# Kernel tuning notes

Hardware: AMD Instinct MI355X
Metric: run time of the kernel (lower is better)

Reference implementation:

```python
import jax, jax.numpy as jnp
import numpy as np
import math

IN_DIM = 3
WIDTH = 256
DEPTH = 6
OUT_DIM = 1
W0_FIRST = 30.0
W0_HIDDEN = 1.0
N_POINTS = 1048576


def _uniform(key, shape, bound):
    return jax.random.uniform(key, shape, dtype=jnp.float32, minval=-bound, maxval=bound)


def setup_inputs() -> dict:
    key = jax.random.key(0)
    ks = jax.random.split(key, 8)
    xyt = jax.random.uniform(ks[0], (N_POINTS, IN_DIM), dtype=jnp.float32, minval=-1.0, maxval=1.0)
    # first layer: bound = 1/in_features
    W0 = _uniform(ks[1], (WIDTH, IN_DIM), 1.0 / IN_DIM)
    b0 = jnp.zeros((WIDTH,), jnp.float32)
    # hidden layers: bound = sqrt(6/width)/w0_hidden
    hb = math.sqrt(6.0 / WIDTH) / W0_HIDDEN
    W1 = _uniform(ks[2], (WIDTH, WIDTH), hb)
    b1 = jnp.zeros((WIDTH,), jnp.float32)
    W2 = _uniform(ks[3], (WIDTH, WIDTH), hb)
    b2 = jnp.zeros((WIDTH,), jnp.float32)
    W3 = _uniform(ks[4], (WIDTH, WIDTH), hb)
    b3 = jnp.zeros((WIDTH,), jnp.float32)
    W4 = _uniform(ks[5], (WIDTH, WIDTH), hb)
    b4 = jnp.zeros((WIDTH,), jnp.float32)
    Wf = _uniform(ks[6], (OUT_DIM, WIDTH), hb)
    bf = jnp.zeros((OUT_DIM,), jnp.float32)
    return {"xyt": xyt, "W0": W0, "b0": b0, "W1": W1, "b1": b1,
            "W2": W2, "b2": b2, "W3": W3, "b3": b3, "W4": W4, "b4": b4,
            "Wf": Wf, "bf": bf}


def reference(xyt, W0, b0, W1, b1, W2, b2, W3, b3, W4, b4, Wf, bf):
    # SineLayer: sin(w0 * (x @ W^T + b)); torch Linear weight is [out, in]
    h = jnp.sin(W0_FIRST * (xyt @ W0.T + b0))          # [N, 256]
    for W, b in ((W1, b1), (W2, b2), (W3, b3), (W4, b4)):
        h = jnp.sin(W0_HIDDEN * (h @ W.T + b))          # [N, 256]
    out = h @ Wf.T + bf                                  # [N, 1]
    return out.squeeze(-1)                               # [N]
```

## Files before the change

kernel.cpp:

```cpp
#include <hip/hip_runtime.h>

typedef _Float16 half8 __attribute__((ext_vector_type(8)));
typedef _Float16 half4 __attribute__((ext_vector_type(4)));
typedef float f32x4 __attribute__((ext_vector_type(4)));

#define WPAD 264
#define NPB 128
#define THREADS 512
#define INV2PI 0.15915494309189535f
#define W0SCALE (30.0f * INV2PI)
#define SMEM_BYTES (NPB * WPAD * 2 + (384 + 256) * 4)

__global__ void convert_weights(const float* __restrict__ W1, const float* __restrict__ W2,
                                const float* __restrict__ W3, const float* __restrict__ W4,
                                _Float16* __restrict__ Wc) {
    int tid = blockIdx.x * 256 + threadIdx.x;
    int l   = tid >> 16;
    int rem = tid & 65535;
    int n = rem >> 8, k = rem & 255;
    const float* W = (l == 0) ? W1 : (l == 1) ? W2 : (l == 2) ? W3 : W4;
    int kc = k >> 5, kl = k & 31;
    Wc[l * 65536 + kc * 8192 + n * 32 + kl] = (_Float16)(W[rem] * INV2PI);
}

__launch_bounds__(THREADS, 4)
__global__ void siren_fused(const float* __restrict__ xyt,
                            const float* __restrict__ W0,
                            const float* __restrict__ b0,
                            const _Float16* __restrict__ Wc,
                            const float* __restrict__ b1,
                            const float* __restrict__ b2,
                            const float* __restrict__ b3,
                            const float* __restrict__ b4,
                            const float* __restrict__ Wf,
                            const float* __restrict__ bfin,
                            float* __restrict__ out)
{
    extern __shared__ _Float16 smem[];
    _Float16* hbuf = smem;
    float* xs   = (float*)(smem + NPB * WPAD);
    float* wf_s = xs + 384;

    const int tid  = threadIdx.x;
    const int lane = tid & 63;
    const int wv   = tid >> 6;
    const int l15  = lane & 15;
    const int l4   = lane >> 4;
    const int gm0  = blockIdx.x * NPB;

    if (tid < 384) xs[tid] = xyt[gm0 * 3 + tid];
    if (tid < 256) wf_s[tid] = Wf[tid];
    __syncthreads();

    {
        const int fg = lane;
        const int p0 = wv * 16;
        float w[4][3], bb[4];
        #pragma unroll
        for (int c = 0; c < 4; ++c) {
            const int n = fg * 4 + c;
            w[c][0] = W0[n * 3 + 0] * W0SCALE;
            w[c][1] = W0[n * 3 + 1] * W0SCALE;
            w[c][2] = W0[n * 3 + 2] * W0SCALE;
            bb[c]   = b0[n] * W0SCALE;
        }
        #pragma unroll 4
        for (int p = 0; p < 16; ++p) {
            const float x0 = xs[(p0 + p) * 3], x1 = xs[(p0 + p) * 3 + 1], x2 = xs[(p0 + p) * 3 + 2];
            half4 hv;
            #pragma unroll
            for (int c = 0; c < 4; ++c) {
                float z = fmaf(w[c][0], x0, fmaf(w[c][1], x1, fmaf(w[c][2], x2, bb[c])));
                hv[c] = (_Float16)__builtin_amdgcn_sinf(z);
            }
            *(half4*)&hbuf[(p0 + p) * WPAD + fg * 4] = hv;
        }
    }

    const int arow = (wv * 32 + l15) * 32 + l4 * 8;

    #pragma unroll
    for (int l = 0; l < 4; ++l) {
        const float* bl = (l == 0) ? b1 : (l == 1) ? b2 : (l == 2) ? b3 : b4;
        const _Float16* wl = Wc + l * 65536;

        half8 areg[2][2];
        #pragma unroll
        for (int c = 0; c < 2; ++c)
            #pragma unroll
            for (int i = 0; i < 2; ++i)
                areg[c][i] = *(const half8*)&wl[c * 8192 + arow + i * 512];

        f32x4 acc[2][8];
        #pragma unroll
        for (int i = 0; i < 2; ++i) {
            f32x4 bb = *(const f32x4*)&bl[wv * 32 + i * 16 + l4 * 4];
            bb *= INV2PI;
            #pragma unroll
            for (int j = 0; j < 8; ++j)
                acc[i][j] = bb;
        }

        __syncthreads();

        #pragma unroll
        for (int kc = 0; kc < 8; ++kc) {
            half8 anext[2];
            if (kc < 6) {
                #pragma unroll
                for (int i = 0; i < 2; ++i)
                    anext[i] = *(const half8*)&wl[(kc + 2) * 8192 + arow + i * 512];
            }
            #pragma unroll
            for (int g = 0; g < 2; ++g) {
                half8 bfr[4];
                #pragma unroll
                for (int j = 0; j < 4; ++j)
                    bfr[j] = *(const half8*)&hbuf[((g * 4 + j) * 16 + l15) * WPAD + kc * 32 + l4 * 8];
                #pragma unroll
                for (int i = 0; i < 2; ++i)
                    #pragma unroll
                    for (int j = 0; j < 4; ++j)
                        acc[i][g * 4 + j] = __builtin_amdgcn_mfma_f32_16x16x32_f16(
                            areg[kc & 1][i], bfr[j], acc[i][g * 4 + j], 0, 0, 0);
            }
            if (kc < 6) { areg[kc & 1][0] = anext[0]; areg[kc & 1][1] = anext[1]; }
        }

        __syncthreads();

        #pragma unroll
        for (int i = 0; i < 2; ++i)
            #pragma unroll
            for (int j = 0; j < 8; ++j) {
                half4 hv;
                #pragma unroll
                for (int r = 0; r < 4; ++r)
                    hv[r] = (_Float16)__builtin_amdgcn_sinf(acc[i][j][r]);
                *(half4*)&hbuf[(j * 16 + l15) * WPAD + wv * 32 + i * 16 + l4 * 4] = hv;
            }
    }

    __syncthreads();

    {
        const int m = tid >> 2, q = tid & 3;
        const _Float16* hrow = &hbuf[m * WPAD + q * 64];
        float sum = 0.f;
        #pragma unroll
        for (int i = 0; i < 8; ++i) {
            half8 hv = *(const half8*)&hrow[i * 8];
            const int nb = q * 64 + i * 8;
            #pragma unroll
            for (int j = 0; j < 8; ++j)
                sum = fmaf((float)hv[j], wf_s[nb + j], sum);
        }
        sum += __shfl_down(sum, 2);
        sum += __shfl_down(sum, 1);
        if (q == 0) out[gm0 + m] = sum + bfin[0];
    }
}

extern "C" void kernel_launch(void* const* d_in, const int* in_sizes, int n_in,
                              void* d_out, int out_size, void* d_ws, size_t ws_size,
                              hipStream_t stream) {
    const float* xyt = (const float*)d_in[0];
    const float* W0  = (const float*)d_in[1];
    const float* b0  = (const float*)d_in[2];
    const float* W1  = (const float*)d_in[3];
    const float* b1  = (const float*)d_in[4];
    const float* W2  = (const float*)d_in[5];
    const float* b2  = (const float*)d_in[6];
    const float* W3  = (const float*)d_in[7];
    const float* b3  = (const float*)d_in[8];
    const float* W4  = (const float*)d_in[9];
    const float* b4  = (const float*)d_in[10];
    const float* Wf  = (const float*)d_in[11];
    const float* bf  = (const float*)d_in[12];
    float* out = (float*)d_out;
    _Float16* Wc = (_Float16*)d_ws;

    hipFuncSetAttribute((const void*)siren_fused,
                        hipFuncAttributeMaxDynamicSharedMemorySize, SMEM_BYTES);

    convert_weights<<<1024, 256, 0, stream>>>(W1, W2, W3, W4, Wc);

    const int N = in_sizes[0] / 3;
    siren_fused<<<N / NPB, THREADS, SMEM_BYTES, stream>>>(
        xyt, W0, b0, Wc, b1, b2, b3, b4, Wf, bf, out);
}
```

Measured before the change: 620.6 us.

## Switch to 32x32x16 MFMA with XOR-swizzled unpadded activation buffer

Replaces the 16x16x32 MFMA tiling with 32x32x16 MFMAs, each wave computing a 64-feature by 64-point tile. The activation buffer drops its row padding and uses an XOR swizzle to avoid LDS bank conflicts. Weight fragments are streamed through a four-deep register ring that is prefetched across layer boundaries. Sine outputs are packed with cvt_pkrtz, which rounds toward zero instead of to nearest. The aim is fewer LDS reads per MFMA and better latency hiding, at the cost of more complex indexing and higher register pressure.

```diff
diff --git a/kernel.cpp b/kernel.cpp
--- a/kernel.cpp
+++ b/kernel.cpp
@@ -2,14 +2,25 @@
 
 typedef _Float16 half8 __attribute__((ext_vector_type(8)));
 typedef _Float16 half4 __attribute__((ext_vector_type(4)));
+typedef __fp16  fp16x2 __attribute__((ext_vector_type(2)));
 typedef float f32x4 __attribute__((ext_vector_type(4)));
-
-#define WPAD 264
+typedef float f32x16 __attribute__((ext_vector_type(16)));
+
 #define NPB 128
 #define THREADS 512
 #define INV2PI 0.15915494309189535f
 #define W0SCALE (30.0f * INV2PI)
-#define SMEM_BYTES (NPB * WPAD * 2 + (384 + 256) * 4)
+#define SMEM_BYTES (65536 + 384*4 + 256*4)
+
+
+__device__ __forceinline__ half4 pk4(float a, float b, float c, float d) {
+    fp16x2 lo = __builtin_amdgcn_cvt_pkrtz(a, b);
+    fp16x2 hi = __builtin_amdgcn_cvt_pkrtz(c, d);
+    half4 r;
+    r[0] = (_Float16)lo[0]; r[1] = (_Float16)lo[1];
+    r[2] = (_Float16)hi[0]; r[3] = (_Float16)hi[1];
+    return r;
+}
 
 __global__ void convert_weights(const float* __restrict__ W1, const float* __restrict__ W2,
                                 const float* __restrict__ W3, const float* __restrict__ W4,
@@ -38,14 +49,17 @@
 {
     extern __shared__ _Float16 smem[];
     _Float16* hbuf = smem;
-    float* xs   = (float*)(smem + NPB * WPAD);
+    float* xs   = (float*)(smem + 32768);
     float* wf_s = xs + 384;
 
     const int tid  = threadIdx.x;
     const int lane = tid & 63;
     const int wv   = tid >> 6;
-    const int l15  = lane & 15;
-    const int l4   = lane >> 4;
+    const int fq   = wv & 3;
+    const int ph   = wv >> 2;
+    const int l31  = lane & 31;
+    const int o4   = lane >> 5;
+    const int l7   = lane & 7;
     const int gm0  = blockIdx.x * NPB;
 
     if (tid < 384) xs[tid] = xyt[gm0 * 3 + tid];
@@ -66,78 +80,98 @@
         }
         #pragma unroll 4
         for (int p = 0; p < 16; ++p) {
-            const float x0 = xs[(p0 + p) * 3], x1 = xs[(p0 + p) * 3 + 1], x2 = xs[(p0 + p) * 3 + 2];
-            half4 hv;
-            #pragma unroll
-            for (int c = 0; c < 4; ++c) {
-                float z = fmaf(w[c][0], x0, fmaf(w[c][1], x1, fmaf(w[c][2], x2, bb[c])));
-                hv[c] = (_Float16)__builtin_amdgcn_sinf(z);
-            }
-            *(half4*)&hbuf[(p0 + p) * WPAD + fg * 4] = hv;
-        }
-    }
-
-    const int arow = (wv * 32 + l15) * 32 + l4 * 8;
+            const int pt = p0 + p;
+            const float x0 = xs[pt * 3], x1 = xs[pt * 3 + 1], x2 = xs[pt * 3 + 2];
+            float z0 = fmaf(w[0][0], x0, fmaf(w[0][1], x1, fmaf(w[0][2], x2, bb[0])));
+            float z1 = fmaf(w[1][0], x0, fmaf(w[1][1], x1, fmaf(w[1][2], x2, bb[1])));
+            float z2 = fmaf(w[2][0], x0, fmaf(w[2][1], x1, fmaf(w[2][2], x2, bb[2])));
+            float z3 = fmaf(w[3][0], x0, fmaf(w[3][1], x1, fmaf(w[3][2], x2, bb[3])));
+            half4 hv = pk4(__builtin_amdgcn_sinf(z0), __builtin_amdgcn_sinf(z1),
+                           __builtin_amdgcn_sinf(z2), __builtin_amdgcn_sinf(z3));
+            *(half4*)&hbuf[pt * 256 + (((fg >> 1) ^ (pt & 7)) << 3) + (fg & 1) * 4] = hv;
+        }
+    }
+
+    const int m8  = (l7 & ~1) | (o4 ^ (l7 & 1));
+    const int vb0 = (ph * 64 + l31) * 256;
+    const int vb1 = vb0 + 32 * 256;
+    const int ar0 = (fq * 64 + l31) * 32 + o4 * 8;
+    const int ar1 = ar0 + 32 * 32;
+
+    half8 ring[4][2];
+    {
+        const _Float16* wl = Wc;
+        #pragma unroll
+        for (int s = 0; s < 4; ++s) {
+            ring[s][0] = *(const half8*)&wl[(s >> 1) * 8192 + (s & 1) * 16 + ar0];
+            ring[s][1] = *(const half8*)&wl[(s >> 1) * 8192 + (s & 1) * 16 + ar1];
+        }
+    }
 
     #pragma unroll
     for (int l = 0; l < 4; ++l) {
         const float* bl = (l == 0) ? b1 : (l == 1) ? b2 : (l == 2) ? b3 : b4;
         const _Float16* wl = Wc + l * 65536;
 
-        half8 areg[2][2];
-        #pragma unroll
-        for (int c = 0; c < 2; ++c)
-            #pragma unroll
-            for (int i = 0; i < 2; ++i)
-                areg[c][i] = *(const half8*)&wl[c * 8192 + arow + i * 512];
-
-        f32x4 acc[2][8];
+        f32x16 acc[2][2];
         #pragma unroll
         for (int i = 0; i < 2; ++i) {
-            f32x4 bb = *(const f32x4*)&bl[wv * 32 + i * 16 + l4 * 4];
-            bb *= INV2PI;
-            #pragma unroll
-            for (int j = 0; j < 8; ++j)
-                acc[i][j] = bb;
+            #pragma unroll
+            for (int q = 0; q < 4; ++q) {
+                f32x4 bb = *(const f32x4*)&bl[fq * 64 + i * 32 + q * 8 + o4 * 4];
+                bb *= INV2PI;
+                #pragma unroll
+                for (int r = 0; r < 4; ++r) {
+                    acc[i][0][q * 4 + r] = bb[r];
+                    acc[i][1][q * 4 + r] = bb[r];
+                }
+            }
         }
 
         __syncthreads();
 
         #pragma unroll
-        for (int kc = 0; kc < 8; ++kc) {
-            half8 anext[2];
-            if (kc < 6) {
+        for (int ks = 0; ks < 16; ++ks) {
+            half8 a0 = ring[ks & 3][0];
+            half8 a1 = ring[ks & 3][1];
+            if (ks < 12) {
+                ring[ks & 3][0] = *(const half8*)&wl[((ks + 4) >> 1) * 8192 + ((ks + 4) & 1) * 16 + ar0];
+                ring[ks & 3][1] = *(const half8*)&wl[((ks + 4) >> 1) * 8192 + ((ks + 4) & 1) * 16 + ar1];
+            }
+            const int boff = ((2 * ks) ^ m8) << 3;
+            half8 b0f = *(const half8*)&hbuf[vb0 + boff];
+            half8 b1f = *(const half8*)&hbuf[vb1 + boff];
+            acc[0][0] = __builtin_amdgcn_mfma_f32_32x32x16_f16(a0, b0f, acc[0][0], 0, 0, 0);
+            acc[0][1] = __builtin_amdgcn_mfma_f32_32x32x16_f16(a0, b1f, acc[0][1], 0, 0, 0);
+            acc[1][0] = __builtin_amdgcn_mfma_f32_32x32x16_f16(a1, b0f, acc[1][0], 0, 0, 0);
+            acc[1][1] = __builtin_amdgcn_mfma_f32_32x32x16_f16(a1, b1f, acc[1][1], 0, 0, 0);
+        }
+
+        if (l < 3) {
+            const _Float16* wn = wl + 65536;
+            #pragma unroll
+            for (int s = 0; s < 4; ++s) {
+                ring[s][0] = *(const half8*)&wn[(s >> 1) * 8192 + (s & 1) * 16 + ar0];
+                ring[s][1] = *(const half8*)&wn[(s >> 1) * 8192 + (s & 1) * 16 + ar1];
+            }
+        }
+
+        __syncthreads();
+
+        #pragma unroll
+        for (int i = 0; i < 2; ++i)
+            #pragma unroll
+            for (int j = 0; j < 2; ++j) {
+                const int pt = ph * 64 + j * 32 + l31;
                 #pragma unroll
-                for (int i = 0; i < 2; ++i)
-                    anext[i] = *(const half8*)&wl[(kc + 2) * 8192 + arow + i * 512];
-            }
-            #pragma unroll
-            for (int g = 0; g < 2; ++g) {
-                half8 bfr[4];
-                #pragma unroll
-                for (int j = 0; j < 4; ++j)
-                    bfr[j] = *(const half8*)&hbuf[((g * 4 + j) * 16 + l15) * WPAD + kc * 32 + l4 * 8];
-                #pragma unroll
-                for (int i = 0; i < 2; ++i)
-                    #pragma unroll
-                    for (int j = 0; j < 4; ++j)
-                        acc[i][g * 4 + j] = __builtin_amdgcn_mfma_f32_16x16x32_f16(
-                            areg[kc & 1][i], bfr[j], acc[i][g * 4 + j], 0, 0, 0);
-            }
-            if (kc < 6) { areg[kc & 1][0] = anext[0]; areg[kc & 1][1] = anext[1]; }
-        }
-
-        __syncthreads();
-
-        #pragma unroll
-        for (int i = 0; i < 2; ++i)
-            #pragma unroll
-            for (int j = 0; j < 8; ++j) {
-                half4 hv;
-                #pragma unroll
-                for (int r = 0; r < 4; ++r)
-                    hv[r] = (_Float16)__builtin_amdgcn_sinf(acc[i][j][r]);
-                *(half4*)&hbuf[(j * 16 + l15) * WPAD + wv * 32 + i * 16 + l4 * 4] = hv;
+                for (int q = 0; q < 4; ++q) {
+                    half4 hv = pk4(__builtin_amdgcn_sinf(acc[i][j][q * 4 + 0]),
+                                   __builtin_amdgcn_sinf(acc[i][j][q * 4 + 1]),
+                                   __builtin_amdgcn_sinf(acc[i][j][q * 4 + 2]),
+                                   __builtin_amdgcn_sinf(acc[i][j][q * 4 + 3]));
+                    const int g = fq * 8 + i * 4 + q;
+                    *(half4*)&hbuf[pt * 256 + ((g ^ l7) << 3) + o4 * 4] = hv;
+                }
             }
     }
 
@@ -145,15 +179,14 @@
 
     {
         const int m = tid >> 2, q = tid & 3;
-        const _Float16* hrow = &hbuf[m * WPAD + q * 64];
         float sum = 0.f;
         #pragma unroll
         for (int i = 0; i < 8; ++i) {
-            half8 hv = *(const half8*)&hrow[i * 8];
+            half8 hv = *(const half8*)&hbuf[m * 256 + (((q * 8 + i) ^ (m & 7)) << 3)];
             const int nb = q * 64 + i * 8;
             #pragma unroll
-            for (int j = 0; j < 8; ++j)
-                sum = fmaf((float)hv[j], wf_s[nb + j], sum);
+            for (int jj = 0; jj < 8; ++jj)
+                sum = fmaf((float)hv[jj], wf_s[nb + jj], sum);
         }
         sum += __shfl_down(sum, 2);
         sum += __shfl_down(sum, 1);
@@ -180,7 +213,7 @@
     float* out = (float*)d_out;
     _Float16* Wc = (_Float16*)d_ws;
 
-    hipFuncSetAttribute((const void*)siren_fused,
+    (void)hipFuncSetAttribute((const void*)siren_fused,
                         hipFuncAttributeMaxDynamicSharedMemorySize, SMEM_BYTES);
 
     convert_weights<<<1024, 256, 0, stream>>>(W1, W2, W3, W4, Wc);
```

New measurement: 786.5 us. 26.7% more time.
